# Optimization experiments

Measured on AMD Instinct MI355X. Metric: run time of the kernel, lower is better.

Reference implementation:

```python
import jax, jax.numpy as jnp
import numpy as np

N, E, F_IN, H, NSE, L, C, G = 50000, 800000, 128, 128, 16, 3, 10, 256


def setup_inputs() -> dict:
    key = jax.random.key(0)
    ks = jax.random.split(key, 32)
    sc = 0.05
    inp = {
        "x": jax.random.normal(ks[0], (N, F_IN), jnp.float32),
        "s": jax.random.normal(ks[1], (N, NSE), jnp.float32),
        "edge_index": jax.random.randint(ks[2], (2, E), 0, N, jnp.int64),
        "batch": jnp.sort(jax.random.randint(ks[3], (N,), 0, G, jnp.int64)),
        # pre: Linear(F_IN, H); embedding_s: Linear(NSE, H)
        "pre_w": jax.random.normal(ks[4], (F_IN, H), jnp.float32) * sc,
        "pre_b": jnp.zeros((H,), jnp.float32),
        "emb_w": jax.random.normal(ks[5], (NSE, H), jnp.float32) * sc,
        "emb_b": jnp.zeros((H,), jnp.float32),
        # per-layer GIN MLP: Linear(2H,H) -> ReLU -> Linear(H,H)
        "gin_w1": jax.random.normal(ks[6], (L, 2 * H, H), jnp.float32) * sc,
        "gin_b1": jnp.zeros((L, H), jnp.float32),
        "gin_w2": jax.random.normal(ks[7], (L, H, H), jnp.float32) * sc,
        "gin_b2": jnp.zeros((L, H), jnp.float32),
        # per-layer GCNConv(H, H)
        "gcn_w": jax.random.normal(ks[8], (L, H, H), jnp.float32) * sc,
        "gcn_b": jnp.zeros((L, H), jnp.float32),
        "whp_w": jax.random.normal(ks[9], (2 * H, H), jnp.float32) * sc,
        "whp_b": jnp.zeros((H,), jnp.float32),
        "post_w": jax.random.normal(ks[10], (H, H), jnp.float32) * sc,
        "post_b": jnp.zeros((H,), jnp.float32),
        "ro_w": jax.random.normal(ks[11], (H, C), jnp.float32) * sc,
        "ro_b": jnp.zeros((C,), jnp.float32),
    }
    return inp


def reference(x, s, edge_index, batch, pre_w, pre_b, emb_w, emb_b,
              gin_w1, gin_b1, gin_w2, gin_b2, gcn_w, gcn_b,
              whp_w, whp_b, post_w, post_b, ro_w, ro_b):
    src, dst = edge_index[0], edge_index[1]
    x = x @ pre_w + pre_b                      # [N, H]
    s = s @ emb_w + emb_b                      # [N, H]
    # GCN symmetric norm with self-loops (deg includes the +1 self loop)
    deg = jax.ops.segment_sum(jnp.ones((E,), x.dtype), dst, num_segments=N) + 1.0
    dinv = jax.lax.rsqrt(deg)                  # [N]
    enorm = (dinv[src] * dinv[dst])[:, None]   # [E, 1]
    self_norm = (dinv * dinv)[:, None]         # [N, 1]
    for i in range(L):
        xc = jnp.concatenate([x, s], axis=-1)  # [N, 2H]
        # GINConv (eps=0): nn(x_i + sum_j x_j)
        agg = jax.ops.segment_sum(xc[src], dst, num_segments=N)
        h = xc + agg
        h = jax.nn.relu(h @ gin_w1[i] + gin_b1[i]) @ gin_w2[i] + gin_b2[i]
        x = jax.nn.relu(h)                     # dropout is identity in eval mode
        # GCNConv on s stream
        hs = s @ gcn_w[i]
        sagg = jax.ops.segment_sum(hs[src] * enorm, dst, num_segments=N)
        s = jnp.tanh(sagg + hs * self_norm + gcn_b[i])
    x = jnp.concatenate([x, s], axis=-1) @ whp_w + whp_b
    g = jax.ops.segment_sum(x, batch, num_segments=G)   # global_add_pool [G, H]
    g = jax.nn.relu(g @ post_w + post_b)
    return jax.nn.log_softmax(g @ ro_w + ro_b, axis=1)
```

## Files before the change

kernel.cpp:

```cpp
#include <hip/hip_runtime.h>
#include <math.h>

typedef __attribute__((ext_vector_type(8))) short short8;
typedef __attribute__((ext_vector_type(4))) float f32x4;
typedef unsigned int uint;
typedef unsigned short ushort;

#define HGRID(n, b) (((n) + (b) - 1) / (b))

__device__ __forceinline__ ushort f2bu(float f) {
    uint x = __builtin_bit_cast(uint, f);
    x = (x + 0x7fffu + ((x >> 16) & 1u)) >> 16;
    return (ushort)x;
}
__device__ __forceinline__ float blo(uint u) {
    return __builtin_bit_cast(float, u << 16);
}
__device__ __forceinline__ float bhi(uint u) {
    return __builtin_bit_cast(float, u & 0xffff0000u);
}
__device__ __forceinline__ uint packbf(float a, float b) {
    return (uint)f2bu(a) | ((uint)f2bu(b) << 16);
}

__device__ __forceinline__ void gload16(const void* g, void* l) {
    __builtin_amdgcn_global_load_lds(
        (const __attribute__((address_space(1))) void*)g,
        (__attribute__((address_space(3))) void*)l, 16, 0, 0);
}


__global__ void init_kernel(int* __restrict__ cnt, int* __restrict__ cur,
                            float* __restrict__ gbuf, int N, int GH) {
    int i = blockIdx.x * 256 + threadIdx.x;
    if (i < N) { cnt[i] = 0; cur[i] = 0; }
    if (i < GH) gbuf[i] = 0.f;
}


__global__ void count_kernel(const int* __restrict__ dst, int* __restrict__ cnt, int E) {
    int e = blockIdx.x * 256 + threadIdx.x;
    if (e < E) atomicAdd(&cnt[dst[e]], 1);
}

__global__ void scan_part(const int* __restrict__ cnt, int* __restrict__ bsum, int N) {
    __shared__ int sh[256];
    int b = blockIdx.x, t = threadIdx.x;
    int base = b * 1024 + t * 4;
    int tsum = 0;
    if (base + 3 < N) {
        int4 v = *(const int4*)(cnt + base);
        tsum = v.x + v.y + v.z + v.w;
    } else {
        #pragma unroll
        for (int k = 0; k < 4; ++k) if (base + k < N) tsum += cnt[base + k];
    }
    sh[t] = tsum;
    __syncthreads();
    for (int d = 128; d > 0; d >>= 1) {
        if (t < d) sh[t] += sh[t + d];
        __syncthreads();
    }
    if (t == 0) bsum[b] = sh[0];
}

__global__ void scan_fill(const int* __restrict__ cnt, const int* __restrict__ bsum,
                          int* __restrict__ offs, float* __restrict__ dinv,
                          int N, int E) {
    __shared__ int sh[256];
    __shared__ int sbase;
    int b = blockIdx.x, t = threadIdx.x;

    if (t < 64) {
        int s = 0;
        for (int i = t; i < b; i += 64) s += bsum[i];
        #pragma unroll
        for (int d = 32; d > 0; d >>= 1) s += __shfl_down(s, d, 64);
        if (t == 0) sbase = s;
    }

    int base = b * 1024 + t * 4;
    int c[4] = {0, 0, 0, 0};
    if (base + 3 < N) {
        int4 v = *(const int4*)(cnt + base);
        c[0] = v.x; c[1] = v.y; c[2] = v.z; c[3] = v.w;
    } else {
        #pragma unroll
        for (int k = 0; k < 4; ++k) if (base + k < N) c[k] = cnt[base + k];
    }
    int tsum = c[0] + c[1] + c[2] + c[3];
    sh[t] = tsum;
    __syncthreads();
    for (int d = 1; d < 256; d <<= 1) {
        int o = (t >= d) ? sh[t - d] : 0;
        __syncthreads();
        sh[t] += o;
        __syncthreads();
    }
    int run = sbase + sh[t] - tsum;
    #pragma unroll
    for (int k = 0; k < 4; ++k) {
        if (base + k < N) {
            offs[base + k] = run;
            dinv[base + k] = rsqrtf((float)c[k] + 1.0f);
            run += c[k];
        }
    }
    if (b == 0 && t == 0) offs[N] = E;
}

__global__ void fill_kernel(const int* __restrict__ src, const int* __restrict__ dst,
                            const int* __restrict__ offs, int* __restrict__ cur,
                            const float* __restrict__ dinv, int2* __restrict__ epack, int E) {
    int e = blockIdx.x * 256 + threadIdx.x;
    if (e < E) {
        int d = dst[e];
        int sv = src[e];
        int p = offs[d] + atomicAdd(&cur[d], 1);
        epack[p] = make_int2(sv * 64, __float_as_int(dinv[sv]));
    }
}


struct PrepArgs {
    const float *x, *s;
    const float *pre_w, *pre_b, *emb_w, *emb_b, *gin_w1, *gcn_w, *gin_w2, *whp_w;
    ushort *xs, *Wt_preemb, *Wt_dual, *Wt_gin2, *Wt_whp;
    float *bias_comb;
    int L, N;
};

__global__ void prep_kernel(PrepArgs a) {
    long idx = (long)blockIdx.x * 256 + threadIdx.x;
    long nconv = (long)a.N * 24;
    if (idx < nconv) {
        int n = (int)(idx / 24), ch = (int)(idx % 24);
        uint4 o = {0u, 0u, 0u, 0u};
        if (ch < 16) {
            const float4* px = (const float4*)(a.x + (long)n * 128 + ch * 8);
            float4 u = px[0], v = px[1];
            o.x = packbf(u.x, u.y); o.y = packbf(u.z, u.w);
            o.z = packbf(v.x, v.y); o.w = packbf(v.z, v.w);
        } else if (ch < 18) {
            const float4* ps = (const float4*)(a.s + (long)n * 16 + (ch - 16) * 8);
            float4 u = ps[0], v = ps[1];
            o.x = packbf(u.x, u.y); o.y = packbf(u.z, u.w);
            o.z = packbf(v.x, v.y); o.w = packbf(v.z, v.w);
        }
        *(uint4*)(a.xs + idx * 8) = o;
        return;
    }
    idx -= nconv;
    if (idx < 49152) {
        int c = (int)(idx / 192), k = (int)(idx % 192);
        float v = 0.f;
        if (c < 128) { if (k < 128) v = a.pre_w[(long)k * 128 + c]; }
        else if (k >= 128 && k < 144) v = a.emb_w[(long)(k - 128) * 128 + (c - 128)];
        a.Wt_preemb[idx] = f2bu(v);
        return;
    }
    idx -= 49152;
    if (idx < (long)a.L * 65536) {
        int i = (int)(idx / 65536);
        int r = (int)(idx % 65536);
        int c = r / 256, k = r % 256;
        float v = 0.f;
        if (c < 128) v = a.gin_w1[(long)i * 32768 + (long)k * 128 + c];
        else if (k >= 128) v = a.gcn_w[(long)i * 16384 + (long)(k - 128) * 128 + (c - 128)];
        a.Wt_dual[idx] = f2bu(v);
        return;
    }
    idx -= (long)a.L * 65536;
    if (idx < (long)a.L * 16384) {
        int i = (int)(idx / 16384);
        int r = (int)(idx % 16384);
        int c = r / 128, k = r % 128;
        a.Wt_gin2[idx] = f2bu(a.gin_w2[(long)i * 16384 + (long)k * 128 + c]);
        return;
    }
    idx -= (long)a.L * 16384;
    if (idx < 32768) {
        int c = (int)(idx / 256), k = (int)(idx % 256);
        a.Wt_whp[idx] = f2bu(a.whp_w[(long)k * 128 + c]);
        return;
    }
    idx -= 32768;
    if (idx < 256) a.bias_comb[idx] = (idx < 128) ? a.pre_b[idx] : a.emb_b[idx - 128];
}


template<int KPAD, int BN>
__global__ __launch_bounds__(512) void lin_mfma(
    const ushort* __restrict__ A, int a_stride,
    const ushort* __restrict__ Wt, const float* __restrict__ bias,
    ushort* __restrict__ out, int o_stride, int N, int act, int interleaved)
{
    constexpr int BK = 64;
    constexpr int NF = BN / 64;
    __shared__ __align__(16) ushort LA[128][BK];
    __shared__ __align__(16) ushort LB[BN][BK];

    const int tid  = threadIdx.x;
    const int l    = tid & 63;
    const int w    = tid >> 6;
    const int wr   = w >> 2;
    const int wc   = w & 3;
    const int row0 = blockIdx.x * 128;
    const int l15  = l & 15;
    const int lhi  = l >> 4;
    const int lrow = l >> 3;
    const int lslot = l & 7;

    f32x4 acc[4][NF];
    #pragma unroll
    for (int m = 0; m < 4; ++m)
        #pragma unroll
        for (int n = 0; n < NF; ++n) acc[m][n] = (f32x4){0.f, 0.f, 0.f, 0.f};

    for (int k0 = 0; k0 < KPAD; k0 += BK) {
        __syncthreads();
        #pragma unroll
        for (int i = 0; i < 2; ++i) {
            int ci = w * 2 + i;
            int r  = ci * 8 + lrow;
            int gr = row0 + r; if (gr > N - 1) gr = N - 1;
            gload16(A + (long)gr * a_stride + k0 + ((lslot ^ (r & 7)) * 8), &LA[ci * 8][0]);
        }
        #pragma unroll
        for (int i = 0; i < NF; ++i) {
            int ci = w * NF + i;
            int c  = ci * 8 + lrow;
            gload16(Wt + (long)c * KPAD + k0 + ((lslot ^ (c & 7)) * 8), &LB[ci * 8][0]);
        }
        __syncthreads();
        #pragma unroll
        for (int kk = 0; kk < BK; kk += 32) {
            int chb = (kk >> 3) + lhi;
            short8 a[4];
            #pragma unroll
            for (int m = 0; m < 4; ++m) {
                int r = wr * 64 + m * 16 + l15;
                a[m] = *(const short8*)&LA[r][(chb ^ (r & 7)) * 8];
            }
            #pragma unroll
            for (int n = 0; n < NF; ++n) {
                int c = wc * (BN / 4) + n * 16 + l15;
                short8 b = *(const short8*)&LB[c][(chb ^ (c & 7)) * 8];
                #pragma unroll
                for (int m = 0; m < 4; ++m)
                    acc[m][n] = __builtin_amdgcn_mfma_f32_16x16x32_bf16(a[m], b, acc[m][n], 0, 0, 0);
            }
        }
    }

    #pragma unroll
    for (int n = 0; n < NF; ++n) {
        int col = wc * (BN / 4) + n * 16 + l15;
        float bv = bias ? bias[col] : 0.f;
        #pragma unroll
        for (int m = 0; m < 4; ++m) {
            #pragma unroll
            for (int j = 0; j < 4; ++j) {
                int gr = row0 + wr * 64 + m * 16 + (lhi << 2) + j;
                if (gr < N) {
                    float v = acc[m][n][j] + bv;
                    if (act) v = fmaxf(v, 0.f);
                    long off;
                    if (interleaved) {
                        int cc = col & 127;
                        off = (long)gr * 256 + 4 * (cc >> 1) + ((col >> 7) << 1) + (cc & 1);
                    } else {
                        off = (long)gr * o_stride + col;
                    }
                    out[off] = f2bu(v);
                }
            }
        }
    }
}


__global__ __launch_bounds__(256) void fused_gather(
    const uint2* __restrict__ yh, const int* __restrict__ offs,
    const int2* __restrict__ epack,
    const float* __restrict__ dinv,
    const float* __restrict__ b1, const float* __restrict__ gb,
    uint* __restrict__ h1p, uint* __restrict__ xcp, int N)
{
    int node = blockIdx.x * 4 + (threadIdx.x >> 6);
    if (node >= N) return;
    node = __builtin_amdgcn_readfirstlane(node);
    int l = threadIdx.x & 63;

    uint2 self = yh[(long)node * 64 + l];
    float di = dinv[node];
    float g0 = blo(self.x), g1 = bhi(self.x);
    float s0 = 0.f, s1 = 0.f;

    int j0 = __builtin_amdgcn_readfirstlane(offs[node]);
    int j1 = __builtin_amdgcn_readfirstlane(offs[node + 1]);
    int jmid = j0 + ((j1 - j0) & ~7);

    for (int j = j0; j < jmid; j += 8) {
        int2 e[8]; uint2 v[8];
        #pragma unroll
        for (int k = 0; k < 8; ++k) e[k] = epack[j + k];
        #pragma unroll
        for (int k = 0; k < 8; ++k) v[k] = yh[e[k].x + l];
        #pragma unroll
        for (int k = 0; k < 8; ++k) {
            float ds = __int_as_float(e[k].y);
            g0 += blo(v[k].x);
            g1 += bhi(v[k].x);
            s0 += blo(v[k].y) * ds;
            s1 += bhi(v[k].y) * ds;
        }
    }
    if (jmid < j1) {
        int2 e[8]; uint2 v[8];
        #pragma unroll
        for (int k = 0; k < 8; ++k) {
            int jj = jmid + k;
            e[k] = epack[(jj < j1) ? jj : (j1 - 1)];
            if (jj >= j1) e[k].y = 0;
        }
        #pragma unroll
        for (int k = 0; k < 8; ++k) v[k] = yh[e[k].x + l];
        #pragma unroll
        for (int k = 0; k < 8; ++k) {
            float ds = __int_as_float(e[k].y);
            float m = (jmid + k < j1) ? 1.f : 0.f;
            g0 += blo(v[k].x) * m;
            g1 += bhi(v[k].x) * m;
            s0 += blo(v[k].y) * ds;
            s1 += bhi(v[k].y) * ds;
        }
    }

    float2 bb = ((const float2*)b1)[l];
    g0 = fmaxf(g0 + bb.x, 0.f);
    g1 = fmaxf(g1 + bb.y, 0.f);
    h1p[(long)node * 64 + l] = packbf(g0, g1);

    float dii = di * di;
    float2 gg = ((const float2*)gb)[l];
    float t0 = tanhf(s0 * di + blo(self.y) * dii + gg.x);
    float t1 = tanhf(s1 * di + bhi(self.y) * dii + gg.y);
    xcp[(long)node * 128 + 64 + l] = packbf(t0, t1);
}


__global__ void pool_kernel(const ushort* __restrict__ xh, const int* __restrict__ batch,
                            float* __restrict__ g, int N) {
    int c  = threadIdx.x;
    int n0 = blockIdx.x * 128;
    if (n0 >= N) return;
    int n1 = min(n0 + 128, N);
    int curg = batch[n0];
    float acc = 0.f;
    for (int n = n0; n < n1; ++n) {
        int b = batch[n];
        if (b != curg) {
            atomicAdd(&g[(long)curg * 128 + c], acc);
            acc = 0.f;
            curg = b;
        }
        acc += blo((uint)xh[(long)n * 128 + c]);
    }
    atomicAdd(&g[(long)curg * 128 + c], acc);
}


__global__ void head_kernel(const float* __restrict__ g, const float* __restrict__ post_w,
                            const float* __restrict__ post_b, const float* __restrict__ ro_w,
                            const float* __restrict__ ro_b, float* __restrict__ out, int C) {
    __shared__ float row[128];
    __shared__ float g2[128];
    __shared__ float lg[16];
    __shared__ float s_lse;
    int gi = blockIdx.x;
    int c  = threadIdx.x;
    row[c] = g[(long)gi * 128 + c];
    __syncthreads();
    float acc = post_b[c];
    for (int k = 0; k < 128; ++k) acc += row[k] * post_w[k * 128 + c];
    g2[c] = fmaxf(acc, 0.f);
    __syncthreads();
    if (c < C) {
        float a = ro_b[c];
        for (int k = 0; k < 128; ++k) a += g2[k] * ro_w[k * C + c];
        lg[c] = a;
    }
    __syncthreads();
    if (c == 0) {
        float m = lg[0];
        for (int i = 1; i < C; ++i) m = fmaxf(m, lg[i]);
        float sum = 0.f;
        for (int i = 0; i < C; ++i) sum += expf(lg[i] - m);
        s_lse = m + logf(sum);
    }
    __syncthreads();
    if (c < C) out[(long)gi * C + c] = lg[c] - s_lse;
}


extern "C" void kernel_launch(void* const* d_in, const int* in_sizes, int n_in,
                              void* d_out, int out_size, void* d_ws, size_t ws_size,
                              hipStream_t stream) {
    const float* x      = (const float*)d_in[0];
    const float* s_in   = (const float*)d_in[1];
    const int*   ei     = (const int*)d_in[2];
    const int*   batch  = (const int*)d_in[3];
    const float* pre_w  = (const float*)d_in[4];
    const float* pre_b  = (const float*)d_in[5];
    const float* emb_w  = (const float*)d_in[6];
    const float* emb_b  = (const float*)d_in[7];
    const float* gin_w1 = (const float*)d_in[8];
    const float* gin_b1 = (const float*)d_in[9];
    const float* gin_w2 = (const float*)d_in[10];
    const float* gin_b2 = (const float*)d_in[11];
    const float* gcn_w  = (const float*)d_in[12];
    const float* gcn_b  = (const float*)d_in[13];
    const float* whp_w  = (const float*)d_in[14];
    const float* whp_b  = (const float*)d_in[15];
    const float* post_w = (const float*)d_in[16];
    const float* post_b = (const float*)d_in[17];
    const float* ro_w   = (const float*)d_in[18];
    const float* ro_b   = (const float*)d_in[19];

    const int H = 128;
    const int N = in_sizes[0] / 128;
    const int E = in_sizes[2] / 2;
    const int C = in_sizes[19];
    const int G = out_size / C;
    const int L = in_sizes[9] / H;

    const int* srcv = ei;
    const int* dstv = ei + E;

    char* p = (char*)d_ws;
    auto alloc = [&](size_t bytes) -> void* {
        void* r = (void*)p;
        p += (bytes + 255) & ~(size_t)255;
        return r;
    };
    ushort* xc   = (ushort*)alloc((size_t)N * 256 * 2);
    ushort* yh   = (ushort*)alloc((size_t)N * 256 * 2);
    ushort* h1   = (ushort*)alloc((size_t)N * 128 * 2);
    ushort* xs   = (ushort*)alloc((size_t)N * 192 * 2);
    ushort* ybuf = (ushort*)alloc((size_t)N * 128 * 2);
    ushort* Wt_preemb = (ushort*)alloc(256 * 192 * 2);
    ushort* Wt_dual   = (ushort*)alloc((size_t)L * 256 * 256 * 2);
    ushort* Wt_gin2   = (ushort*)alloc((size_t)L * 128 * 128 * 2);
    ushort* Wt_whp    = (ushort*)alloc(128 * 256 * 2);
    float*  bias_comb = (float*)alloc(256 * 4);
    float*  dinv = (float*)alloc((size_t)N * 4);
    float*  gbuf = (float*)alloc((size_t)G * 128 * 4);
    int* cnt   = (int*)alloc((size_t)N * 4);
    int* offs  = (int*)alloc((size_t)(N + 1) * 4);
    int* cur   = (int*)alloc((size_t)N * 4);
    int* bsum  = (int*)alloc((size_t)HGRID(N, 1024) * 4);
    int2* epack = (int2*)alloc((size_t)E * 8);

    const int nb = HGRID(N, 1024);

    init_kernel<<<HGRID(N, 256), 256, 0, stream>>>(cnt, cur, gbuf, N, G * 128);
    count_kernel<<<HGRID(E, 256), 256, 0, stream>>>(dstv, cnt, E);
    scan_part<<<nb, 256, 0, stream>>>(cnt, bsum, N);
    scan_fill<<<nb, 256, 0, stream>>>(cnt, bsum, offs, dinv, N, E);
    fill_kernel<<<HGRID(E, 256), 256, 0, stream>>>(srcv, dstv, offs, cur, dinv, epack, E);

    PrepArgs pa;
    pa.x = x; pa.s = s_in;
    pa.pre_w = pre_w; pa.pre_b = pre_b; pa.emb_w = emb_w; pa.emb_b = emb_b;
    pa.gin_w1 = gin_w1; pa.gcn_w = gcn_w; pa.gin_w2 = gin_w2; pa.whp_w = whp_w;
    pa.xs = xs; pa.Wt_preemb = Wt_preemb; pa.Wt_dual = Wt_dual; pa.Wt_gin2 = Wt_gin2;
    pa.Wt_whp = Wt_whp; pa.bias_comb = bias_comb; pa.L = L; pa.N = N;
    long prep_tot = (long)N * 24 + 49152 + (long)L * 65536 + (long)L * 16384 + 32768 + 256;
    prep_kernel<<<HGRID(prep_tot, 256), 256, 0, stream>>>(pa);

    const int lb = HGRID(N, 128);
    lin_mfma<192, 256><<<lb, 512, 0, stream>>>(xs, 192, Wt_preemb, bias_comb,
                                               xc, 256, N, 0, 0);

    for (int i = 0; i < L; ++i) {
        lin_mfma<256, 256><<<lb, 512, 0, stream>>>(xc, 256, Wt_dual + (size_t)i * 65536,
                                                   nullptr, yh, 256, N, 0, 1);
        fused_gather<<<HGRID(N, 4), 256, 0, stream>>>(
            (const uint2*)yh, offs, epack, dinv,
            gin_b1 + (size_t)i * H, gcn_b + (size_t)i * H,
            (uint*)h1, (uint*)xc, N);
        lin_mfma<128, 128><<<lb, 512, 0, stream>>>(h1, 128, Wt_gin2 + (size_t)i * 16384,
                                                   gin_b2 + (size_t)i * H, xc, 256, N, 1, 0);
    }

    lin_mfma<256, 128><<<lb, 512, 0, stream>>>(xc, 256, Wt_whp, whp_b, ybuf, 128, N, 0, 0);

    pool_kernel<<<HGRID(N, 128), 128, 0, stream>>>(ybuf, batch, gbuf, N);
    head_kernel<<<G, 128, 0, stream>>>(gbuf, post_w, post_b, ro_w, ro_b, (float*)d_out, C);
}
```

Measured before the change: 431.1 us.

## Pool before the whp linear layer and widen the gather unroll to 16

```diff
diff --git a/kernel.cpp b/kernel.cpp
--- a/kernel.cpp
+++ b/kernel.cpp
@@ -31,10 +31,12 @@
 
 
 __global__ void init_kernel(int* __restrict__ cnt, int* __restrict__ cur,
-                            float* __restrict__ gbuf, int N, int GH) {
+                            float* __restrict__ gsum, int* __restrict__ cntg,
+                            int N, int GH, int G) {
     int i = blockIdx.x * 256 + threadIdx.x;
     if (i < N) { cnt[i] = 0; cur[i] = 0; }
-    if (i < GH) gbuf[i] = 0.f;
+    if (i < GH) gsum[i] = 0.f;
+    if (i < G) cntg[i] = 0;
 }
 
 
@@ -124,8 +126,8 @@
 
 struct PrepArgs {
     const float *x, *s;
-    const float *pre_w, *pre_b, *emb_w, *emb_b, *gin_w1, *gcn_w, *gin_w2, *whp_w;
-    ushort *xs, *Wt_preemb, *Wt_dual, *Wt_gin2, *Wt_whp;
+    const float *pre_w, *pre_b, *emb_w, *emb_b, *gin_w1, *gcn_w, *gin_w2;
+    ushort *xs, *Wt_preemb, *Wt_dual, *Wt_gin2;
     float *bias_comb;
     int L, N;
 };
@@ -179,12 +181,6 @@
         return;
     }
     idx -= (long)a.L * 16384;
-    if (idx < 32768) {
-        int c = (int)(idx / 256), k = (int)(idx % 256);
-        a.Wt_whp[idx] = f2bu(a.whp_w[(long)k * 128 + c]);
-        return;
-    }
-    idx -= 32768;
     if (idx < 256) a.bias_comb[idx] = (idx < 128) ? a.pre_b[idx] : a.emb_b[idx - 128];
 }
 
@@ -299,16 +295,16 @@
 
     int j0 = __builtin_amdgcn_readfirstlane(offs[node]);
     int j1 = __builtin_amdgcn_readfirstlane(offs[node + 1]);
-    int jmid = j0 + ((j1 - j0) & ~7);
-
-    for (int j = j0; j < jmid; j += 8) {
-        int2 e[8]; uint2 v[8];
-        #pragma unroll
-        for (int k = 0; k < 8; ++k) e[k] = epack[j + k];
-        #pragma unroll
-        for (int k = 0; k < 8; ++k) v[k] = yh[e[k].x + l];
-        #pragma unroll
-        for (int k = 0; k < 8; ++k) {
+    int jmid = j0 + ((j1 - j0) & ~15);
+
+    for (int j = j0; j < jmid; j += 16) {
+        int2 e[16]; uint2 v[16];
+        #pragma unroll
+        for (int k = 0; k < 16; ++k) e[k] = epack[j + k];
+        #pragma unroll
+        for (int k = 0; k < 16; ++k) v[k] = yh[e[k].x + l];
+        #pragma unroll
+        for (int k = 0; k < 16; ++k) {
             float ds = __int_as_float(e[k].y);
             g0 += blo(v[k].x);
             g1 += bhi(v[k].x);
@@ -316,11 +312,11 @@
             s1 += bhi(v[k].y) * ds;
         }
     }
-    if (jmid < j1) {
+    for (int j = jmid; j < j1; j += 8) {
         int2 e[8]; uint2 v[8];
         #pragma unroll
         for (int k = 0; k < 8; ++k) {
-            int jj = jmid + k;
+            int jj = j + k;
             e[k] = epack[(jj < j1) ? jj : (j1 - 1)];
             if (jj >= j1) e[k].y = 0;
         }
@@ -329,7 +325,7 @@
         #pragma unroll
         for (int k = 0; k < 8; ++k) {
             float ds = __int_as_float(e[k].y);
-            float m = (jmid + k < j1) ? 1.f : 0.f;
+            float m = (j + k < j1) ? 1.f : 0.f;
             g0 += blo(v[k].x) * m;
             g1 += bhi(v[k].x) * m;
             s0 += blo(v[k].y) * ds;
@@ -350,41 +346,54 @@
 }
 
 
-__global__ void pool_kernel(const ushort* __restrict__ xh, const int* __restrict__ batch,
-                            float* __restrict__ g, int N) {
+__global__ void pool_kernel(const ushort* __restrict__ xc, const int* __restrict__ batch,
+                            float* __restrict__ gsum, int* __restrict__ cntg, int N) {
     int c  = threadIdx.x;
     int n0 = blockIdx.x * 128;
     if (n0 >= N) return;
     int n1 = min(n0 + 128, N);
     int curg = batch[n0];
     float acc = 0.f;
+    int cnt = 0;
     for (int n = n0; n < n1; ++n) {
         int b = batch[n];
         if (b != curg) {
-            atomicAdd(&g[(long)curg * 128 + c], acc);
-            acc = 0.f;
+            atomicAdd(&gsum[(long)curg * 256 + c], acc);
+            if (c == 0) atomicAdd(&cntg[curg], cnt);
+            acc = 0.f; cnt = 0;
             curg = b;
         }
-        acc += blo((uint)xh[(long)n * 128 + c]);
-    }
-    atomicAdd(&g[(long)curg * 128 + c], acc);
-}
-
-
-__global__ void head_kernel(const float* __restrict__ g, const float* __restrict__ post_w,
-                            const float* __restrict__ post_b, const float* __restrict__ ro_w,
-                            const float* __restrict__ ro_b, float* __restrict__ out, int C) {
-    __shared__ float row[128];
+        acc += blo((uint)xc[(long)n * 256 + c]);
+        cnt++;
+    }
+    atomicAdd(&gsum[(long)curg * 256 + c], acc);
+    if (c == 0) atomicAdd(&cntg[curg], cnt);
+}
+
+
+__global__ void head_kernel(const float* __restrict__ gsum, const int* __restrict__ cntg,
+                            const float* __restrict__ whp_w, const float* __restrict__ whp_b,
+                            const float* __restrict__ post_w, const float* __restrict__ post_b,
+                            const float* __restrict__ ro_w, const float* __restrict__ ro_b,
+                            float* __restrict__ out, int C) {
+    __shared__ float row[256];
+    __shared__ float xr[128];
     __shared__ float g2[128];
     __shared__ float lg[16];
     __shared__ float s_lse;
     int gi = blockIdx.x;
     int c  = threadIdx.x;
-    row[c] = g[(long)gi * 128 + c];
-    __syncthreads();
-    float acc = post_b[c];
-    for (int k = 0; k < 128; ++k) acc += row[k] * post_w[k * 128 + c];
-    g2[c] = fmaxf(acc, 0.f);
+    row[c]       = gsum[(long)gi * 256 + c];
+    row[c + 128] = gsum[(long)gi * 256 + 128 + c];
+    __syncthreads();
+    float cntf = (float)cntg[gi];
+    float acc = cntf * whp_b[c];
+    for (int k = 0; k < 256; ++k) acc += row[k] * whp_w[(long)k * 128 + c];
+    xr[c] = acc;
+    __syncthreads();
+    float a2 = post_b[c];
+    for (int k = 0; k < 128; ++k) a2 += xr[k] * post_w[k * 128 + c];
+    g2[c] = fmaxf(a2, 0.f);
     __syncthreads();
     if (c < C) {
         float a = ro_b[c];
@@ -448,14 +457,13 @@
     ushort* yh   = (ushort*)alloc((size_t)N * 256 * 2);
     ushort* h1   = (ushort*)alloc((size_t)N * 128 * 2);
     ushort* xs   = (ushort*)alloc((size_t)N * 192 * 2);
-    ushort* ybuf = (ushort*)alloc((size_t)N * 128 * 2);
     ushort* Wt_preemb = (ushort*)alloc(256 * 192 * 2);
     ushort* Wt_dual   = (ushort*)alloc((size_t)L * 256 * 256 * 2);
     ushort* Wt_gin2   = (ushort*)alloc((size_t)L * 128 * 128 * 2);
-    ushort* Wt_whp    = (ushort*)alloc(128 * 256 * 2);
     float*  bias_comb = (float*)alloc(256 * 4);
     float*  dinv = (float*)alloc((size_t)N * 4);
-    float*  gbuf = (float*)alloc((size_t)G * 128 * 4);
+    float*  gsum = (float*)alloc((size_t)G * 256 * 4);
+    int*    cntg = (int*)alloc((size_t)G * 4);
     int* cnt   = (int*)alloc((size_t)N * 4);
     int* offs  = (int*)alloc((size_t)(N + 1) * 4);
     int* cur   = (int*)alloc((size_t)N * 4);
@@ -464,7 +472,8 @@
 
     const int nb = HGRID(N, 1024);
 
-    init_kernel<<<HGRID(N, 256), 256, 0, stream>>>(cnt, cur, gbuf, N, G * 128);
+    init_kernel<<<HGRID(max(N, G * 256), 256), 256, 0, stream>>>(cnt, cur, gsum, cntg,
+                                                                 N, G * 256, G);
     count_kernel<<<HGRID(E, 256), 256, 0, stream>>>(dstv, cnt, E);
     scan_part<<<nb, 256, 0, stream>>>(cnt, bsum, N);
     scan_fill<<<nb, 256, 0, stream>>>(cnt, bsum, offs, dinv, N, E);
@@ -473,10 +482,10 @@
     PrepArgs pa;
     pa.x = x; pa.s = s_in;
     pa.pre_w = pre_w; pa.pre_b = pre_b; pa.emb_w = emb_w; pa.emb_b = emb_b;
-    pa.gin_w1 = gin_w1; pa.gcn_w = gcn_w; pa.gin_w2 = gin_w2; pa.whp_w = whp_w;
+    pa.gin_w1 = gin_w1; pa.gcn_w = gcn_w; pa.gin_w2 = gin_w2;
     pa.xs = xs; pa.Wt_preemb = Wt_preemb; pa.Wt_dual = Wt_dual; pa.Wt_gin2 = Wt_gin2;
-    pa.Wt_whp = Wt_whp; pa.bias_comb = bias_comb; pa.L = L; pa.N = N;
-    long prep_tot = (long)N * 24 + 49152 + (long)L * 65536 + (long)L * 16384 + 32768 + 256;
+    pa.bias_comb = bias_comb; pa.L = L; pa.N = N;
+    long prep_tot = (long)N * 24 + 49152 + (long)L * 65536 + (long)L * 16384 + 256;
     prep_kernel<<<HGRID(prep_tot, 256), 256, 0, stream>>>(pa);
 
     const int lb = HGRID(N, 128);
@@ -494,8 +503,7 @@
                                                    gin_b2 + (size_t)i * H, xc, 256, N, 1, 0);
     }
 
-    lin_mfma<256, 128><<<lb, 512, 0, stream>>>(xc, 256, Wt_whp, whp_b, ybuf, 128, N, 0, 0);
-
-    pool_kernel<<<HGRID(N, 128), 128, 0, stream>>>(ybuf, batch, gbuf, N);
-    head_kernel<<<G, 128, 0, stream>>>(gbuf, post_w, post_b, ro_w, ro_b, (float*)d_out, C);
-}
+    pool_kernel<<<HGRID(N, 128), 256, 0, stream>>>(xc, batch, gsum, cntg, N);
+    head_kernel<<<G, 128, 0, stream>>>(gsum, cntg, whp_w, whp_b,
+                                       post_w, post_b, ro_w, ro_b, (float*)d_out, C);
+}
```

Result: no change. 423.6 us (-1.7%).
